# Optimization experiments

Hardware: AMD Instinct MI355X
Metric: run time of the kernel (lower is better)

Reference implementation:

```python
import jax, jax.numpy as jnp
import numpy as np

B, M, D = 512, 32, 64
LAYERS = [128, 128, 128]


def _cin_layer(h, x0, W, b):
    # h: [B, H, D], x0: [B, M, D], W: [O, H*M] (1x1 conv weight squeezed), b: [O]
    O = W.shape[0]
    H = h.shape[1]
    Wr = W.reshape(O, H, M)
    # fused outer-product + 1x1 conv: z[b,h,m,d] = h[b,h,d]*x0[b,m,d]; out = W @ z
    out = jnp.einsum('bhd,bmd,ohm->bod', h, x0, Wr) + b[None, :, None]
    return jax.nn.relu(out)


def setup_inputs() -> dict:
    key = jax.random.key(0)
    ks = jax.random.split(key, 10)
    inp = {"input": jax.random.normal(ks[0], (B, M, D), dtype=jnp.float32)}
    H = M
    fan_scales = []
    Ws, bs = [], []
    for i, O in enumerate(LAYERS):
        cin = H * M
        s = 1.0 / np.sqrt(cin)
        Ws.append(jax.random.uniform(ks[1 + 2 * i], (O, cin), minval=-s, maxval=s, dtype=jnp.float32))
        bs.append(jax.random.uniform(ks[2 + 2 * i], (O,), minval=-s, maxval=s, dtype=jnp.float32))
        H = O  # direct=True
    out_dim = sum(LAYERS)
    s = 1.0 / np.sqrt(out_dim)
    inp.update({"W0": Ws[0], "b0": bs[0], "W1": Ws[1], "b1": bs[1], "W2": Ws[2], "b2": bs[2]})
    inp["lw"] = jax.random.uniform(ks[7], (1, out_dim), minval=-s, maxval=s, dtype=jnp.float32)
    inp["lb"] = jax.random.uniform(ks[8], (1,), minval=-s, maxval=s, dtype=jnp.float32)
    return inp


def reference(input, W0, b0, W1, b1, W2, b2, lw, lb):
    x0 = input  # [B, M, D]
    h = x0
    finals = []
    for W, b in ((W0, b0), (W1, b1), (W2, b2)):
        h = _cin_layer(h, x0, W, b)  # direct=True: output feeds both next hidden and final
        finals.append(h)
    result = jnp.concatenate(finals, axis=1)          # [B, sum(layers), D]
    result = jnp.sum(result, axis=-1)                  # [B, sum(layers)]
    score = result @ lw.T + lb                         # [B, 1]
    return score.squeeze(-1)                           # [B]
```

## Files before the change

kernel.cpp:

```cpp
#include <hip/hip_runtime.h>


constexpr int Bb = 512, Mm = 32, Dd = 64, Oo = 128;

typedef __attribute__((ext_vector_type(8))) short bf16x8;
typedef __attribute__((ext_vector_type(4))) float f32x4;

static __device__ __forceinline__ ushort f2bf(float f) {
  union { float f; uint u; } v;
  v.f = f;
  uint u = v.u;
  return (ushort)((u + 0x7FFFu + ((u >> 16) & 1u)) >> 16);
}
static __device__ __forceinline__ float bf2f(ushort b) {
  union { uint u; float f; } v;
  v.u = (uint)b << 16;
  return v.f;
}

static __device__ __forceinline__ void wsplit_one(const float* __restrict__ W,
                                                  ushort* __restrict__ Whi,
                                                  ushort* __restrict__ Wlo,
                                                  int H, int t) {
  int l = t & 63, fo = (t >> 6) & 7, hh = t >> 9;
  int o = fo * 16 + (l & 15);
  int m0 = (l >> 4) * 8;
  const float* src = W + (size_t)o * (H * 32) + hh * 32 + m0;
  ushort hi[8], lo[8];
#pragma unroll
  for (int j = 0; j < 8; ++j) {
    float w = src[j];
    ushort h = f2bf(w);
    hi[j] = h;
    lo[j] = f2bf(w - bf2f(h));
  }
  *reinterpret_cast<uint4*>(Whi + (size_t)t * 8) = *reinterpret_cast<uint4*>(hi);
  *reinterpret_cast<uint4*>(Wlo + (size_t)t * 8) = *reinterpret_cast<uint4*>(lo);
}

static __device__ __forceinline__ void x0split_one(const float* __restrict__ x0,
                                                   ushort* __restrict__ Xhi,
                                                   ushort* __restrict__ Xlo, int t) {
  int l = t & 63, fd = (t >> 6) & 3, b = t >> 8;
  int d = fd * 16 + (l & 15);
  int m0 = (l >> 4) * 8;
  const float* src = x0 + ((size_t)b * Mm + m0) * Dd + d;
  ushort hi[8], lo[8];
#pragma unroll
  for (int j = 0; j < 8; ++j) {
    float w = src[j * Dd];
    ushort h = f2bf(w);
    hi[j] = h;
    lo[j] = f2bf(w - bf2f(h));
  }
  *reinterpret_cast<uint4*>(Xhi + (size_t)t * 8) = *reinterpret_cast<uint4*>(hi);
  *reinterpret_cast<uint4*>(Xlo + (size_t)t * 8) = *reinterpret_cast<uint4*>(lo);
}

__global__ __launch_bounds__(256) void prep_kernel(
    const float* __restrict__ W0, const float* __restrict__ W1,
    const float* __restrict__ W2, const float* __restrict__ x0,
    ushort* __restrict__ Whi0, ushort* __restrict__ Wlo0,
    ushort* __restrict__ Whi1, ushort* __restrict__ Wlo1,
    ushort* __restrict__ Whi2, ushort* __restrict__ Wlo2,
    ushort* __restrict__ Xhi, ushort* __restrict__ Xlo) {
  int t = blockIdx.x * 256 + threadIdx.x;
  if (t < 16384) {
    wsplit_one(W0, Whi0, Wlo0, 32, t);
  } else if (t < 81920) {
    wsplit_one(W1, Whi1, Wlo1, 128, t - 16384);
  } else if (t < 147456) {
    wsplit_one(W2, Whi2, Wlo2, 128, t - 81920);
  } else {
    x0split_one(x0, Xhi, Xlo, t - 147456);
  }
}

template <int H, bool WRITE_H>
static __device__ __forceinline__ void run_layer(
    const float* __restrict__ h_lds,
    float* __restrict__ h_next,
    const ushort* __restrict__ Whi, const ushort* __restrict__ Wlo,
    const float* __restrict__ bias, const float* __restrict__ lw,
    const bf16x8 (&xh)[4], const bf16x8 (&xl)[4],
    int f, int lane, float& score_part) {
  const int cid = lane & 15;
  const size_t hstride = (size_t)8 * 64 * 8;
  const ushort* pwh = Whi + ((size_t)f * 64 + lane) * 8;
  const ushort* pwl = Wlo + ((size_t)f * 64 + lane) * 8;

  const f32x4 kZ = {0.f, 0.f, 0.f, 0.f};
  f32x4 acc[4];
#pragma unroll
  for (int fd = 0; fd < 4; ++fd) acc[fd] = kZ;

  bf16x8 Ah[3], Al[3];
#pragma unroll
  for (int j = 0; j < 3; ++j) {
    Ah[j] = *reinterpret_cast<const bf16x8*>(pwh + (size_t)j * hstride);
    Al[j] = *reinterpret_cast<const bf16x8*>(pwl + (size_t)j * hstride);
  }
  float hvc[4];
#pragma unroll
  for (int fd = 0; fd < 4; ++fd) hvc[fd] = h_lds[fd * 16 + cid];

#pragma unroll 1
  for (int hh3 = 0; hh3 < H; hh3 += 3) {
#pragma unroll
    for (int j = 0; j < 3; ++j) {
      const int hh = hh3 + j;
      if (H % 3 != 0 && hh >= H) break;
      const int hn1 = (hh + 1 < H) ? hh + 1 : H - 1;
      float nhv[4];
#pragma unroll
      for (int fd = 0; fd < 4; ++fd) nhv[fd] = h_lds[hn1 * 64 + fd * 16 + cid];

      f32x4 y[4];
#pragma unroll
      for (int fd = 0; fd < 4; ++fd)
        y[fd] = __builtin_amdgcn_mfma_f32_16x16x32_bf16(Ah[j], xh[fd], kZ, 0, 0, 0);
#pragma unroll
      for (int fd = 0; fd < 4; ++fd)
        y[fd] = __builtin_amdgcn_mfma_f32_16x16x32_bf16(Ah[j], xl[fd], y[fd], 0, 0, 0);
#pragma unroll
      for (int fd = 0; fd < 4; ++fd)
        y[fd] = __builtin_amdgcn_mfma_f32_16x16x32_bf16(Al[j], xh[fd], y[fd], 0, 0, 0);

      const int hn3 = (hh + 3 < H) ? hh + 3 : H - 1;
      Ah[j] = *reinterpret_cast<const bf16x8*>(pwh + (size_t)hn3 * hstride);
      Al[j] = *reinterpret_cast<const bf16x8*>(pwl + (size_t)hn3 * hstride);

#pragma unroll
      for (int fd = 0; fd < 4; ++fd)
#pragma unroll
        for (int r = 0; r < 4; ++r)
          acc[fd][r] = fmaf(hvc[fd], y[fd][r], acc[fd][r]);
#pragma unroll
      for (int fd = 0; fd < 4; ++fd) hvc[fd] = nhv[fd];
    }
  }

  const int rg = lane >> 4;
#pragma unroll
  for (int r = 0; r < 4; ++r) {
    const int o = f * 16 + rg * 4 + r;
    const float bs = bias[o];
    float sd = 0.f;
#pragma unroll
    for (int fd = 0; fd < 4; ++fd) {
      float v = acc[fd][r] + bs;
      v = v > 0.f ? v : 0.f;
      if (WRITE_H) h_next[o * 64 + fd * 16 + cid] = v;
      sd += v;
    }
#pragma unroll
    for (int mk = 1; mk < 16; mk <<= 1) sd += __shfl_xor(sd, mk, 64);
    if (cid == 0) score_part = fmaf(sd, lw[o], score_part);
  }
}

__global__ __launch_bounds__(512, 2) void cin_fused_kernel(
    const float* __restrict__ x0,
    const ushort* __restrict__ Whi0, const ushort* __restrict__ Wlo0,
    const ushort* __restrict__ Whi1, const ushort* __restrict__ Wlo1,
    const ushort* __restrict__ Whi2, const ushort* __restrict__ Wlo2,
    const ushort* __restrict__ Xhi, const ushort* __restrict__ Xlo,
    const float* __restrict__ b0, const float* __restrict__ b1,
    const float* __restrict__ b2, const float* __restrict__ lw,
    const float* __restrict__ lb, float* __restrict__ out) {
  __shared__ float hA[Oo * Dd];
  __shared__ float hB[Oo * Dd];
  __shared__ float sred[8];

  const int b = blockIdx.x;
  const int t = threadIdx.x;
  const int lane = t & 63;
  const int f = __builtin_amdgcn_readfirstlane(t >> 6);

  reinterpret_cast<float4*>(hA)[t] =
      reinterpret_cast<const float4*>(x0 + (size_t)b * Mm * Dd)[t];

  bf16x8 xh[4], xl[4];
#pragma unroll
  for (int fd = 0; fd < 4; ++fd) {
    size_t off = (((size_t)b * 4 + fd) * 64 + lane) * 8;
    xh[fd] = *reinterpret_cast<const bf16x8*>(Xhi + off);
    xl[fd] = *reinterpret_cast<const bf16x8*>(Xlo + off);
  }

  __syncthreads();

  float score_part = 0.f;
  run_layer<32, true>(hA, hB, Whi0, Wlo0, b0, lw, xh, xl, f, lane, score_part);
  __syncthreads();
  run_layer<128, true>(hB, hA, Whi1, Wlo1, b1, lw + 128, xh, xl, f, lane, score_part);
  __syncthreads();
  run_layer<128, false>(hA, hB, Whi2, Wlo2, b2, lw + 256, xh, xl, f, lane, score_part);

#pragma unroll
  for (int mk = 1; mk < 64; mk <<= 1) score_part += __shfl_xor(score_part, mk, 64);
  if (lane == 0) sred[f] = score_part;
  __syncthreads();
  if (t == 0) {
    float tot = 0.f;
#pragma unroll
    for (int i = 0; i < 8; ++i) tot += sred[i];
    out[b] = tot + lb[0];
  }
}

extern "C" void kernel_launch(void* const* d_in, const int* in_sizes, int n_in,
                              void* d_out, int out_size, void* d_ws, size_t ws_size,
                              hipStream_t stream) {
  const float* x0 = (const float*)d_in[0];
  const float* W0 = (const float*)d_in[1];
  const float* b0 = (const float*)d_in[2];
  const float* W1 = (const float*)d_in[3];
  const float* b1 = (const float*)d_in[4];
  const float* W2 = (const float*)d_in[5];
  const float* b2 = (const float*)d_in[6];
  const float* lw = (const float*)d_in[7];
  const float* lb = (const float*)d_in[8];
  float* out = (float*)d_out;

  ushort* Whi0 = (ushort*)d_ws;
  ushort* Wlo0 = Whi0 + (size_t)32 * 8 * 64 * 8;
  ushort* Whi1 = Wlo0 + (size_t)32 * 8 * 64 * 8;
  ushort* Wlo1 = Whi1 + (size_t)128 * 8 * 64 * 8;
  ushort* Whi2 = Wlo1 + (size_t)128 * 8 * 64 * 8;
  ushort* Wlo2 = Whi2 + (size_t)128 * 8 * 64 * 8;
  ushort* Xhi = Wlo2 + (size_t)128 * 8 * 64 * 8;
  ushort* Xlo = Xhi + (size_t)Bb * 4 * 64 * 8;

  prep_kernel<<<dim3(1088), dim3(256), 0, stream>>>(W0, W1, W2, x0, Whi0, Wlo0,
                                                    Whi1, Wlo1, Whi2, Wlo2, Xhi, Xlo);

  cin_fused_kernel<<<dim3(Bb), dim3(512), 0, stream>>>(
      x0, Whi0, Wlo0, Whi1, Wlo1, Whi2, Wlo2, Xhi, Xlo, b0, b1, b2, lw, lb, out);
}
```

Baseline: 251.4 us.

## Split reduction over H across two wave groups with LDS partial-sum combine

Doubles the block to 1024 threads. The two halves of the waves each process half of the H (hidden-channel) reduction for every layer. One half writes its partial accumulators to LDS, and the other adds them, applies bias and ReLU, and writes the next hidden state. The aim is more waves per CU, to hide MFMA and load latency. The cost is extra barriers, an LDS round trip per layer, and tighter register limits from the raised launch bounds.

```diff
diff --git a/kernel.cpp b/kernel.cpp
--- a/kernel.cpp
+++ b/kernel.cpp
@@ -76,90 +76,109 @@
   }
 }
 
+template <int HW>
+static __device__ __forceinline__ void mfma_loop(
+    const float* __restrict__ hsrc,
+    const ushort* __restrict__ pwh, const ushort* __restrict__ pwl,
+    const bf16x8 (&xh)[4], const bf16x8 (&xl)[4], int cid, f32x4 (&acc)[4]) {
+  const size_t hstride = (size_t)8 * 64 * 8;
+  const f32x4 kZ = {0.f, 0.f, 0.f, 0.f};
+
+  bf16x8 Ah[3], Al[3];
+#pragma unroll
+  for (int j = 0; j < 3; ++j) {
+    Ah[j] = *reinterpret_cast<const bf16x8*>(pwh + (size_t)j * hstride);
+    Al[j] = *reinterpret_cast<const bf16x8*>(pwl + (size_t)j * hstride);
+  }
+  float hvc[4];
+#pragma unroll
+  for (int fd = 0; fd < 4; ++fd) hvc[fd] = hsrc[fd * 16 + cid];
+
+#pragma unroll 1
+  for (int hh3 = 0; hh3 < HW; hh3 += 3) {
+#pragma unroll
+    for (int j = 0; j < 3; ++j) {
+      const int hh = hh3 + j;
+      if (HW % 3 != 0 && hh >= HW) break;
+      const int hn1 = (hh + 1 < HW) ? hh + 1 : HW - 1;
+      float nhv[4];
+#pragma unroll
+      for (int fd = 0; fd < 4; ++fd) nhv[fd] = hsrc[hn1 * 64 + fd * 16 + cid];
+
+      f32x4 y[4];
+#pragma unroll
+      for (int fd = 0; fd < 4; ++fd)
+        y[fd] = __builtin_amdgcn_mfma_f32_16x16x32_bf16(Ah[j], xh[fd], kZ, 0, 0, 0);
+#pragma unroll
+      for (int fd = 0; fd < 4; ++fd)
+        y[fd] = __builtin_amdgcn_mfma_f32_16x16x32_bf16(Ah[j], xl[fd], y[fd], 0, 0, 0);
+#pragma unroll
+      for (int fd = 0; fd < 4; ++fd)
+        y[fd] = __builtin_amdgcn_mfma_f32_16x16x32_bf16(Al[j], xh[fd], y[fd], 0, 0, 0);
+
+      const int hn3 = (hh + 3 < HW) ? hh + 3 : HW - 1;
+      Ah[j] = *reinterpret_cast<const bf16x8*>(pwh + (size_t)hn3 * hstride);
+      Al[j] = *reinterpret_cast<const bf16x8*>(pwl + (size_t)hn3 * hstride);
+
+#pragma unroll
+      for (int fd = 0; fd < 4; ++fd)
+#pragma unroll
+        for (int r = 0; r < 4; ++r) acc[fd][r] = fmaf(hvc[fd], y[fd][r], acc[fd][r]);
+#pragma unroll
+      for (int fd = 0; fd < 4; ++fd) hvc[fd] = nhv[fd];
+    }
+  }
+}
+
 template <int H, bool WRITE_H>
-static __device__ __forceinline__ void run_layer(
-    const float* __restrict__ h_lds,
-    float* __restrict__ h_next,
+static __device__ __forceinline__ void layer(
+    const float* __restrict__ h_src, float* __restrict__ h_next,
     const ushort* __restrict__ Whi, const ushort* __restrict__ Wlo,
     const float* __restrict__ bias, const float* __restrict__ lw,
     const bf16x8 (&xh)[4], const bf16x8 (&xl)[4],
-    int f, int lane, float& score_part) {
+    int f, int kh, int lane, float& score) {
   const int cid = lane & 15;
-  const size_t hstride = (size_t)8 * 64 * 8;
-  const ushort* pwh = Whi + ((size_t)f * 64 + lane) * 8;
-  const ushort* pwl = Wlo + ((size_t)f * 64 + lane) * 8;
-
-  const f32x4 kZ = {0.f, 0.f, 0.f, 0.f};
+  const int rg = lane >> 4;
+  const int hh0 = kh * (H / 2);
+
   f32x4 acc[4];
 #pragma unroll
-  for (int fd = 0; fd < 4; ++fd) acc[fd] = kZ;
-
-  bf16x8 Ah[3], Al[3];
-#pragma unroll
-  for (int j = 0; j < 3; ++j) {
-    Ah[j] = *reinterpret_cast<const bf16x8*>(pwh + (size_t)j * hstride);
-    Al[j] = *reinterpret_cast<const bf16x8*>(pwl + (size_t)j * hstride);
-  }
-  float hvc[4];
-#pragma unroll
-  for (int fd = 0; fd < 4; ++fd) hvc[fd] = h_lds[fd * 16 + cid];
-
-#pragma unroll 1
-  for (int hh3 = 0; hh3 < H; hh3 += 3) {
-#pragma unroll
-    for (int j = 0; j < 3; ++j) {
-      const int hh = hh3 + j;
-      if (H % 3 != 0 && hh >= H) break;
-      const int hn1 = (hh + 1 < H) ? hh + 1 : H - 1;
-      float nhv[4];
-#pragma unroll
-      for (int fd = 0; fd < 4; ++fd) nhv[fd] = h_lds[hn1 * 64 + fd * 16 + cid];
-
-      f32x4 y[4];
-#pragma unroll
-      for (int fd = 0; fd < 4; ++fd)
-        y[fd] = __builtin_amdgcn_mfma_f32_16x16x32_bf16(Ah[j], xh[fd], kZ, 0, 0, 0);
-#pragma unroll
-      for (int fd = 0; fd < 4; ++fd)
-        y[fd] = __builtin_amdgcn_mfma_f32_16x16x32_bf16(Ah[j], xl[fd], y[fd], 0, 0, 0);
-#pragma unroll
-      for (int fd = 0; fd < 4; ++fd)
-        y[fd] = __builtin_amdgcn_mfma_f32_16x16x32_bf16(Al[j], xh[fd], y[fd], 0, 0, 0);
-
-      const int hn3 = (hh + 3 < H) ? hh + 3 : H - 1;
-      Ah[j] = *reinterpret_cast<const bf16x8*>(pwh + (size_t)hn3 * hstride);
-      Al[j] = *reinterpret_cast<const bf16x8*>(pwl + (size_t)hn3 * hstride);
-
-#pragma unroll
-      for (int fd = 0; fd < 4; ++fd)
-#pragma unroll
-        for (int r = 0; r < 4; ++r)
-          acc[fd][r] = fmaf(hvc[fd], y[fd][r], acc[fd][r]);
-#pragma unroll
-      for (int fd = 0; fd < 4; ++fd) hvc[fd] = nhv[fd];
+  for (int fd = 0; fd < 4; ++fd) acc[fd] = (f32x4){0.f, 0.f, 0.f, 0.f};
+
+  const ushort* pwh = Whi + (((size_t)hh0 * 8 + f) * 64 + lane) * 8;
+  const ushort* pwl = Wlo + (((size_t)hh0 * 8 + f) * 64 + lane) * 8;
+  mfma_loop<H / 2>(h_src + hh0 * 64, pwh, pwl, xh, xl, cid, acc);
+
+  if (kh) {
+#pragma unroll
+    for (int r = 0; r < 4; ++r)
+#pragma unroll
+      for (int fd = 0; fd < 4; ++fd)
+        h_next[(f * 16 + rg * 4 + r) * 64 + fd * 16 + cid] = acc[fd][r];
+  }
+  __syncthreads();
+  if (!kh) {
+#pragma unroll
+    for (int r = 0; r < 4; ++r) {
+      const int o = f * 16 + rg * 4 + r;
+      const float bs = bias[o];
+      float sd = 0.f;
+#pragma unroll
+      for (int fd = 0; fd < 4; ++fd) {
+        float v = acc[fd][r] + h_next[o * 64 + fd * 16 + cid] + bs;
+        v = v > 0.f ? v : 0.f;
+        if (WRITE_H) h_next[o * 64 + fd * 16 + cid] = v;
+        sd += v;
+      }
+#pragma unroll
+      for (int mk = 1; mk < 16; mk <<= 1) sd += __shfl_xor(sd, mk, 64);
+      if (cid == 0) score = fmaf(sd, lw[o], score);
     }
   }
-
-  const int rg = lane >> 4;
-#pragma unroll
-  for (int r = 0; r < 4; ++r) {
-    const int o = f * 16 + rg * 4 + r;
-    const float bs = bias[o];
-    float sd = 0.f;
-#pragma unroll
-    for (int fd = 0; fd < 4; ++fd) {
-      float v = acc[fd][r] + bs;
-      v = v > 0.f ? v : 0.f;
-      if (WRITE_H) h_next[o * 64 + fd * 16 + cid] = v;
-      sd += v;
-    }
-#pragma unroll
-    for (int mk = 1; mk < 16; mk <<= 1) sd += __shfl_xor(sd, mk, 64);
-    if (cid == 0) score_part = fmaf(sd, lw[o], score_part);
-  }
-}
-
-__global__ __launch_bounds__(512, 2) void cin_fused_kernel(
+  __syncthreads();
+}
+
+__global__ __launch_bounds__(1024, 4) void cin_fused_kernel(
     const float* __restrict__ x0,
     const ushort* __restrict__ Whi0, const ushort* __restrict__ Wlo0,
     const ushort* __restrict__ Whi1, const ushort* __restrict__ Wlo1,
@@ -170,15 +189,13 @@
     const float* __restrict__ lb, float* __restrict__ out) {
   __shared__ float hA[Oo * Dd];
   __shared__ float hB[Oo * Dd];
-  __shared__ float sred[8];
 
   const int b = blockIdx.x;
   const int t = threadIdx.x;
   const int lane = t & 63;
-  const int f = __builtin_amdgcn_readfirstlane(t >> 6);
-
-  reinterpret_cast<float4*>(hA)[t] =
-      reinterpret_cast<const float4*>(x0 + (size_t)b * Mm * Dd)[t];
+  const int w = __builtin_amdgcn_readfirstlane(t >> 6);
+  const int f = w & 7;
+  const int kh = w >> 3;
 
   bf16x8 xh[4], xl[4];
 #pragma unroll
@@ -188,23 +205,24 @@
     xl[fd] = *reinterpret_cast<const bf16x8*>(Xlo + off);
   }
 
-  __syncthreads();
-
-  float score_part = 0.f;
-  run_layer<32, true>(hA, hB, Whi0, Wlo0, b0, lw, xh, xl, f, lane, score_part);
-  __syncthreads();
-  run_layer<128, true>(hB, hA, Whi1, Wlo1, b1, lw + 128, xh, xl, f, lane, score_part);
-  __syncthreads();
-  run_layer<128, false>(hA, hB, Whi2, Wlo2, b2, lw + 256, xh, xl, f, lane, score_part);
-
-#pragma unroll
-  for (int mk = 1; mk < 64; mk <<= 1) score_part += __shfl_xor(score_part, mk, 64);
-  if (lane == 0) sred[f] = score_part;
+  if (t < 512)
+    reinterpret_cast<float4*>(hA)[t] =
+        reinterpret_cast<const float4*>(x0 + (size_t)b * Mm * Dd)[t];
+  __syncthreads();
+
+  float score = 0.f;
+  layer<32, true>(hA, hB, Whi0, Wlo0, b0, lw, xh, xl, f, kh, lane, score);
+  layer<128, true>(hB, hA, Whi1, Wlo1, b1, lw + 128, xh, xl, f, kh, lane, score);
+  layer<128, false>(hA, hB, Whi2, Wlo2, b2, lw + 256, xh, xl, f, kh, lane, score);
+
+#pragma unroll
+  for (int mk = 1; mk < 64; mk <<= 1) score += __shfl_xor(score, mk, 64);
+  if (lane == 0 && kh == 0) hB[f] = score;
   __syncthreads();
   if (t == 0) {
     float tot = 0.f;
 #pragma unroll
-    for (int i = 0; i < 8; ++i) tot += sred[i];
+    for (int i = 0; i < 8; ++i) tot += hB[i];
     out[b] = tot + lb[0];
   }
 }
@@ -235,6 +253,6 @@
   prep_kernel<<<dim3(1088), dim3(256), 0, stream>>>(W0, W1, W2, x0, Whi0, Wlo0,
                                                     Whi1, Wlo1, Whi2, Wlo2, Xhi, Xlo);
 
-  cin_fused_kernel<<<dim3(Bb), dim3(512), 0, stream>>>(
+  cin_fused_kernel<<<dim3(Bb), dim3(1024), 0, stream>>>(
       x0, Whi0, Wlo0, Whi1, Wlo1, Whi2, Wlo2, Xhi, Xlo, b0, b1, b2, lw, lb, out);
 }
```

Result: no change. 252.6 us (+0.5%).
